# Kernel optimization log

Hardware: AMD Instinct MI355X
Metric: run time of the kernel (lower is better)

The kernel has to match this reference:

```python
import jax, jax.numpy as jnp
import numpy as np

N_NODES = 50000


def setup_inputs() -> dict:
    key = jax.random.key(0)
    ks = jax.random.split(key, 9)
    d = 256
    E = 800000
    inp = {
        "x": jax.random.normal(ks[0], (N_NODES, d), dtype=jnp.float32),
        "edge_index": jax.random.randint(ks[1], (2, E), 0, N_NODES, dtype=jnp.int64),
    }
    # 3 GCNConv layers, each: weight [in, out] and bias [out] (Glorot-ish scale)
    scale = 1.0 / np.sqrt(d)
    for i in range(3):
        inp[f"W{i+1}"] = jax.random.normal(ks[2 + 2 * i], (d, d), dtype=jnp.float32) * scale
        inp[f"b{i+1}"] = jnp.zeros((d,), dtype=jnp.float32)
    return inp


def _gcn_conv(h, src, dst, norm, W, b, n_nodes):
    # linear transform then normalized gather-scatter aggregation
    h = h @ W                                   # [N, out]
    msg = h[src] * norm[:, None]                # [E+N, out]
    out = jax.ops.segment_sum(msg, dst, num_segments=n_nodes)
    return out + b


def reference(x, edge_index, W1, b1, W2, b2, W3, b3):
    n = x.shape[0]
    loop = jnp.arange(n, dtype=edge_index.dtype)
    src = jnp.concatenate([edge_index[0], loop])  # add self-loops
    dst = jnp.concatenate([edge_index[1], loop])
    # symmetric normalization: deg^{-1/2}[src] * deg^{-1/2}[dst]
    deg = jax.ops.segment_sum(jnp.ones_like(dst, dtype=x.dtype), dst, num_segments=n)
    dinv = jnp.where(deg > 0, jax.lax.rsqrt(deg), 0.0)
    norm = dinv[src] * dinv[dst]

    h = _gcn_conv(x, src, dst, norm, W1, b1, n)
    h = jax.nn.relu(h)
    h = _gcn_conv(h, src, dst, norm, W2, b2, n)
    h = jax.nn.relu(h)
    h = _gcn_conv(h, src, dst, norm, W3, b3, n)
    return h
```

## Files before the change

kernel.cpp:

```cpp
#include <hip/hip_runtime.h>
#include <math.h>


using f16x8   = __attribute__((ext_vector_type(8))) _Float16;
using ushort4v = __attribute__((ext_vector_type(4))) unsigned short;
using f32x4   = __attribute__((ext_vector_type(4))) float;
using half4   = __attribute__((ext_vector_type(4))) _Float16;

__device__ inline unsigned short f2h_bits(float v) {
    _Float16 h = (_Float16)v;
    union { _Float16 h; unsigned short u; } c; c.h = h;
    return c.u;
}


__global__ void hist_kernel(const int* __restrict__ dst, int E, int* __restrict__ cnt) {
    int e = blockIdx.x * blockDim.x + threadIdx.x;
    if (e < E) atomicAdd(&cnt[dst[e]], 1);
}

__global__ void scan_block_kernel(const int* __restrict__ in, int n,
                                  int* __restrict__ out, int* __restrict__ bsums) {
    __shared__ int s[256];
    int t = threadIdx.x;
    int i = blockIdx.x * 256 + t;
    s[t] = (i < n) ? in[i] : 0;
    __syncthreads();
    for (int off = 1; off < 256; off <<= 1) {
        int addv = (t >= off) ? s[t - off] : 0;
        __syncthreads();
        s[t] += addv;
        __syncthreads();
    }
    if (i < n) out[i] = s[t];
    if (t == 255) bsums[blockIdx.x] = s[255];
}

__global__ void scan_sums_kernel(int* __restrict__ bsums, int nb) {
    __shared__ int s[256];
    int t = threadIdx.x;
    s[t] = (t < nb) ? bsums[t] : 0;
    __syncthreads();
    for (int off = 1; off < 256; off <<= 1) {
        int addv = (t >= off) ? s[t - off] : 0;
        __syncthreads();
        s[t] += addv;
        __syncthreads();
    }
    if (t < nb) bsums[t] = s[t];
}

__global__ void scan_add_dinv_kernel(int* __restrict__ scn, int n, const int* __restrict__ bsums,
                                     const int* __restrict__ cnt, float* __restrict__ dinv,
                                     int* __restrict__ cursor) {
    int i = blockIdx.x * 256 + threadIdx.x;
    if (i < n) {
        int s = scn[i] + (blockIdx.x > 0 ? bsums[blockIdx.x - 1] : 0);
        scn[i] = s;
        int c = cnt[i];
        dinv[i] = rsqrtf((float)(c + 1));
        cursor[i] = s - c;
    }
}

__global__ void scatter_kernel(const int* __restrict__ src, const int* __restrict__ dst, int E,
                               const float* __restrict__ dinv, int* __restrict__ cursor,
                               int* __restrict__ ssrc, float* __restrict__ snorm) {
    int e = blockIdx.x * blockDim.x + threadIdx.x;
    if (e < E) {
        int s = src[e], d0 = dst[e];
        int pos = atomicAdd(&cursor[d0], 1);
        ssrc[pos] = s;
        snorm[pos] = dinv[s] * dinv[d0];
    }
}

__global__ __launch_bounds__(256) void wsplit3_kernel(const float* __restrict__ Wa,
                                                      const float* __restrict__ Wb,
                                                      const float* __restrict__ Wc,
                                                      unsigned short* __restrict__ Wsp) {
    __shared__ float t[64][65];
    int w = blockIdx.z;
    const float* W = (w == 0) ? Wa : (w == 1) ? Wb : Wc;
    int k0 = blockIdx.x * 64, n0 = blockIdx.y * 64;
    int tid = threadIdx.x;
    int r = tid >> 6, c = tid & 63;
#pragma unroll
    for (int i = 0; i < 16; ++i) {
        int kk = i * 4 + r;
        t[kk][c] = W[(size_t)(k0 + kk) * 256 + n0 + c];
    }
    __syncthreads();
    unsigned short* Hi = Wsp + (size_t)w * 131072;
    unsigned short* Lo = Hi + 65536;
#pragma unroll
    for (int i = 0; i < 16; ++i) {
        int nn = i * 4 + r;
        float v = t[c][nn];
        _Float16 hh = (_Float16)v;
        float rr = v - (float)hh;
        _Float16 ll = (_Float16)rr;
        union { _Float16 h; unsigned short u; } ch, cl; ch.h = hh; cl.h = ll;
        Hi[(size_t)(n0 + nn) * 256 + k0 + c] = ch.u;
        Lo[(size_t)(n0 + nn) * 256 + k0 + c] = cl.u;
    }
}

__global__ void xcast_kernel(const float* __restrict__ in, unsigned short* __restrict__ out16,
                             int total4) {
    int i = blockIdx.x * blockDim.x + threadIdx.x;
    int stride = gridDim.x * blockDim.x;
    for (; i < total4; i += stride) {
        float4 v = ((const float4*)in)[i];
        ushort4v o;
        o[0] = f2h_bits(v.x); o[1] = f2h_bits(v.y);
        o[2] = f2h_bits(v.z); o[3] = f2h_bits(v.w);
        ((ushort4v*)out16)[i] = o;
    }
}

__global__ __launch_bounds__(256) void gemm_f16_kernel(
        const unsigned short* __restrict__ Af, const unsigned short* __restrict__ Whf,
        const unsigned short* __restrict__ Wlf, unsigned short* __restrict__ C16, int M) {
    __shared__ unsigned short lds[24576];

    const int tid  = threadIdx.x;
    const int lane = tid & 63;
    const int wid  = tid >> 6;
    const int wr   = wid >> 1, wc = wid & 1;

    const int orig = blockIdx.x;
    const int xcd  = orig & 7;
    const int idx  = orig >> 3;
    const int wg   = (xcd < 6 ? xcd * 98 : 588 + (xcd - 6) * 97) + idx;
    const int mBase = (wg >> 1) * 128;
    const int nBase = (wg & 1) * 128;

    const int b0 = (lane ^ (lane >> 2) ^ (lane >> 4)) & 1;
    const int b1 = ((lane >> 1) ^ (lane >> 3)) & 1;
    const int b2 = ((lane >> 2) ^ (lane >> 4)) & 1;
    const int g  = (lane & 0x38) | (b2 << 2) | (b1 << 1) | b0;
    const int srow = g >> 2;
    const int skg  = g & 3;

    const unsigned short* cptr[6];
    int cdst[6];
#pragma unroll
    for (int i = 0; i < 6; ++i) {
        int c = wid * 6 + i;
        int a = c >> 3;
        int s = c & 7;
        const unsigned short* base = (a == 0) ? Af : (a == 1) ? Whf : Wlf;
        int rb = (a == 0) ? mBase : nBase;
        int r = rb + s * 16 + srow;
        if (a == 0 && r >= M) r = M - 1;
        cptr[i] = base + (size_t)r * 256 + skg * 8;
        cdst[i] = a * 4096 + s * 512;
    }

    f32x4 acc[4][4];
#pragma unroll
    for (int i = 0; i < 4; ++i)
#pragma unroll
        for (int j = 0; j < 4; ++j) acc[i][j] = (f32x4){0.f, 0.f, 0.f, 0.f};

    auto stage = [&](int p, int k) {
        unsigned short* dbase = lds + p * 12288;
        const int k0 = k * 32;
#pragma unroll
        for (int i = 0; i < 6; ++i) {
            __builtin_amdgcn_global_load_lds(
                (const __attribute__((address_space(1))) void*)(cptr[i] + k0),
                (__attribute__((address_space(3))) void*)(dbase + cdst[i]),
                16, 0, 0);
        }
    };

    stage(0, 0);

#pragma unroll
    for (int k = 0; k < 8; ++k) {
        const int p = k & 1;
        if (k < 7) {
            stage(p ^ 1, k + 1);
            asm volatile("s_waitcnt vmcnt(6)" ::: "memory");
        } else {
            asm volatile("s_waitcnt vmcnt(0)" ::: "memory");
        }
        __builtin_amdgcn_s_barrier();

        const unsigned short* As = lds + p * 12288;
        const unsigned short* Bh = As + 4096;
        const unsigned short* Bl = As + 8192;

        const int kb = (lane >> 4) * 8;
        f16x8 fa[4], fbh[4], fbl[4];
#pragma unroll
        for (int mi = 0; mi < 4; ++mi) {
            int row = wr * 64 + mi * 16 + (lane & 15);
            int off = (row * 64 + kb * 2) ^ ((row & 7) << 4);
            fa[mi] = *(const f16x8*)((const char*)As + off);
        }
#pragma unroll
        for (int ni = 0; ni < 4; ++ni) {
            int col = wc * 64 + ni * 16 + (lane & 15);
            int off = (col * 64 + kb * 2) ^ ((col & 7) << 4);
            fbh[ni] = *(const f16x8*)((const char*)Bh + off);
            fbl[ni] = *(const f16x8*)((const char*)Bl + off);
        }
#pragma unroll
        for (int mi = 0; mi < 4; ++mi)
#pragma unroll
            for (int ni = 0; ni < 4; ++ni) {
                acc[mi][ni] = __builtin_amdgcn_mfma_f32_16x16x32_f16(
                    fa[mi], fbh[ni], acc[mi][ni], 0, 0, 0);
                acc[mi][ni] = __builtin_amdgcn_mfma_f32_16x16x32_f16(
                    fa[mi], fbl[ni], acc[mi][ni], 0, 0, 0);
            }
        __builtin_amdgcn_s_barrier();
    }

#pragma unroll
    for (int mi = 0; mi < 4; ++mi) {
        int row0 = mBase + wr * 64 + mi * 16 + (lane >> 4) * 4;
#pragma unroll
        for (int ni = 0; ni < 4; ++ni) {
            int col = nBase + wc * 64 + ni * 16 + (lane & 15);
#pragma unroll
            for (int r = 0; r < 4; ++r) {
                int row = row0 + r;
                if (row < M) C16[(size_t)row * 256 + col] = f2h_bits(acc[mi][ni][r]);
            }
        }
    }
}

template <int RELU, int SPLIT>
__global__ __launch_bounds__(256) void agg_kernel(const unsigned short* __restrict__ hH,
                                                  const int* __restrict__ ssrc,
                                                  const float* __restrict__ snorm,
                                                  const int* __restrict__ cnt,
                                                  const int* __restrict__ scanv,
                                                  const float* __restrict__ dinv,
                                                  const float* __restrict__ bias,
                                                  unsigned short* __restrict__ outH,
                                                  float* __restrict__ outF, int n) {
    int node = blockIdx.x * 4 + (threadIdx.x >> 6);
    int lane = threadIdx.x & 63;
    if (node >= n) return;
    int end = scanv[node];
    int start = end - cnt[node];
    float di = dinv[node];
    float wself = di * di;

    half4 v = ((const half4*)(hH + (size_t)node * 256))[lane];
    float ax = (float)v[0] * wself, ay = (float)v[1] * wself;
    float az = (float)v[2] * wself, aw = (float)v[3] * wself;

    int j = start;
    for (; j + 4 <= end; j += 4) {
        int s0 = ssrc[j], s1 = ssrc[j + 1], s2 = ssrc[j + 2], s3 = ssrc[j + 3];
        float w0 = snorm[j], w1 = snorm[j + 1], w2 = snorm[j + 2], w3 = snorm[j + 3];
        half4 u0 = ((const half4*)(hH + (size_t)s0 * 256))[lane];
        half4 u1 = ((const half4*)(hH + (size_t)s1 * 256))[lane];
        half4 u2 = ((const half4*)(hH + (size_t)s2 * 256))[lane];
        half4 u3 = ((const half4*)(hH + (size_t)s3 * 256))[lane];
        ax = fmaf((float)u0[0], w0, ax); ay = fmaf((float)u0[1], w0, ay);
        az = fmaf((float)u0[2], w0, az); aw = fmaf((float)u0[3], w0, aw);
        ax = fmaf((float)u1[0], w1, ax); ay = fmaf((float)u1[1], w1, ay);
        az = fmaf((float)u1[2], w1, az); aw = fmaf((float)u1[3], w1, aw);
        ax = fmaf((float)u2[0], w2, ax); ay = fmaf((float)u2[1], w2, ay);
        az = fmaf((float)u2[2], w2, az); aw = fmaf((float)u2[3], w2, aw);
        ax = fmaf((float)u3[0], w3, ax); ay = fmaf((float)u3[1], w3, ay);
        az = fmaf((float)u3[2], w3, az); aw = fmaf((float)u3[3], w3, aw);
    }
    for (; j < end; ++j) {
        int s = ssrc[j];
        float wn = snorm[j];
        half4 u = ((const half4*)(hH + (size_t)s * 256))[lane];
        ax = fmaf((float)u[0], wn, ax); ay = fmaf((float)u[1], wn, ay);
        az = fmaf((float)u[2], wn, az); aw = fmaf((float)u[3], wn, aw);
    }

    float4 bb = ((const float4*)bias)[lane];
    ax += bb.x; ay += bb.y; az += bb.z; aw += bb.w;
    if (RELU) {
        ax = fmaxf(ax, 0.0f); ay = fmaxf(ay, 0.0f);
        az = fmaxf(az, 0.0f); aw = fmaxf(aw, 0.0f);
    }
    if (SPLIT) {
        ushort4v o;
        o[0] = f2h_bits(ax); o[1] = f2h_bits(ay);
        o[2] = f2h_bits(az); o[3] = f2h_bits(aw);
        ((ushort4v*)(outH + (size_t)node * 256))[lane] = o;
    } else {
        float4 o = {ax, ay, az, aw};
        ((float4*)(outF + (size_t)node * 256))[lane] = o;
    }
}

extern "C" void kernel_launch(void* const* d_in, const int* in_sizes, int n_in,
                              void* d_out, int out_size, void* d_ws, size_t ws_size,
                              hipStream_t stream) {
    const float* x  = (const float*)d_in[0];
    const int*   ei = (const int*)d_in[1];
    const float* W1 = (const float*)d_in[2];
    const float* b1 = (const float*)d_in[3];
    const float* W2 = (const float*)d_in[4];
    const float* b2 = (const float*)d_in[5];
    const float* W3 = (const float*)d_in[6];
    const float* b3 = (const float*)d_in[7];

    const int n = in_sizes[0] / 256;
    const int E = in_sizes[1] / 2;
    const int* src = ei;
    const int* dst = ei + E;

    unsigned short* hAct = (unsigned short*)d_out;
    unsigned short* xF   = hAct + (size_t)n * 256;
    float* outF = (float*)d_out;

    char* ws = (char*)d_ws;
    unsigned short* hLin = (unsigned short*)ws;
    size_t off  = (size_t)n * 256 * 2;
    off = (off + 255) & ~(size_t)255;
    float* dinv = (float*)(ws + off); off += (size_t)n * 4;
    int*   cnt  = (int*)(ws + off);   off += (size_t)n * 4;
    int*   scn  = (int*)(ws + off);   off += (size_t)n * 4;
    int*   cur  = (int*)(ws + off);   off += (size_t)n * 4;
    int*   bsum = (int*)(ws + off);   off += 4096;
    int*   ssrc = (int*)(ws + off);   off += (size_t)E * 4;
    float* snrm = (float*)(ws + off); off += (size_t)E * 4;
    off = (off + 255) & ~(size_t)255;
    unsigned short* Wsp = (unsigned short*)(ws + off);
    off += (size_t)3 * 2 * 65536 * 2;

    hipMemsetAsync(cnt, 0, (size_t)n * 4, stream);

    const int eb = (E + 255) / 256;
    const int nb = (n + 255) / 256;

    wsplit3_kernel<<<dim3(4, 4, 3), 256, 0, stream>>>(W1, W2, W3, Wsp);
    xcast_kernel<<<2048, 256, 0, stream>>>(x, xF, n * 64);

    hist_kernel<<<eb, 256, 0, stream>>>(dst, E, cnt);
    scan_block_kernel<<<nb, 256, 0, stream>>>(cnt, n, scn, bsum);
    scan_sums_kernel<<<1, 256, 0, stream>>>(bsum, nb);
    scan_add_dinv_kernel<<<nb, 256, 0, stream>>>(scn, n, bsum, cnt, dinv, cur);
    scatter_kernel<<<eb, 256, 0, stream>>>(src, dst, E, dinv, cur, ssrc, snrm);

    const int gb = ((n + 127) / 128) * 2;
    const int ab = (n + 3) / 4;

    gemm_f16_kernel<<<gb, 256, 0, stream>>>(xF, Wsp, Wsp + 65536, hLin, n);
    agg_kernel<1, 1><<<ab, 256, 0, stream>>>(hLin, ssrc, snrm, cnt, scn, dinv, b1,
                                             hAct, nullptr, n);
    gemm_f16_kernel<<<gb, 256, 0, stream>>>(hAct, Wsp + 131072, Wsp + 196608, hLin, n);
    agg_kernel<1, 1><<<ab, 256, 0, stream>>>(hLin, ssrc, snrm, cnt, scn, dinv, b2,
                                             hAct, nullptr, n);
    gemm_f16_kernel<<<gb, 256, 0, stream>>>(hAct, Wsp + 262144, Wsp + 327680, hLin, n);
    agg_kernel<0, 0><<<ab, 256, 0, stream>>>(hLin, ssrc, snrm, cnt, scn, dinv, b3,
                                             nullptr, outF, n);
}
```

Measured before the change: 355.1 us.

## Widen GEMM tile to full 256 output columns with 512-thread blocks

The f16 GEMM now uses 512-thread blocks that each compute a 128x256 output tile covering all output columns. Each A tile is loaded once rather than twice across two N-halves. LDS per stage grows to hold the full split-precision weight slab. The XCD-aware block remapping is dropped, and the grid halves to 391 blocks, which reduces parallelism and may lower occupancy on the GPU.

```diff
diff --git a/kernel.cpp b/kernel.cpp
--- a/kernel.cpp
+++ b/kernel.cpp
@@ -119,22 +119,17 @@
     }
 }
 
-__global__ __launch_bounds__(256) void gemm_f16_kernel(
+__global__ __launch_bounds__(512) void gemm_f16_kernel(
         const unsigned short* __restrict__ Af, const unsigned short* __restrict__ Whf,
         const unsigned short* __restrict__ Wlf, unsigned short* __restrict__ C16, int M) {
-    __shared__ unsigned short lds[24576];
+    __shared__ unsigned short lds[40960];
 
     const int tid  = threadIdx.x;
     const int lane = tid & 63;
     const int wid  = tid >> 6;
-    const int wr   = wid >> 1, wc = wid & 1;
-
-    const int orig = blockIdx.x;
-    const int xcd  = orig & 7;
-    const int idx  = orig >> 3;
-    const int wg   = (xcd < 6 ? xcd * 98 : 588 + (xcd - 6) * 97) + idx;
-    const int mBase = (wg >> 1) * 128;
-    const int nBase = (wg & 1) * 128;
+    const int wr   = wid >> 2;
+    const int wc   = wid & 3;
+    const int mBase = blockIdx.x * 128;
 
     const int b0 = (lane ^ (lane >> 2) ^ (lane >> 4)) & 1;
     const int b1 = ((lane >> 1) ^ (lane >> 3)) & 1;
@@ -143,19 +138,29 @@
     const int srow = g >> 2;
     const int skg  = g & 3;
 
-    const unsigned short* cptr[6];
-    int cdst[6];
-#pragma unroll
-    for (int i = 0; i < 6; ++i) {
-        int c = wid * 6 + i;
-        int a = c >> 3;
-        int s = c & 7;
-        const unsigned short* base = (a == 0) ? Af : (a == 1) ? Whf : Wlf;
-        int rb = (a == 0) ? mBase : nBase;
-        int r = rb + s * 16 + srow;
-        if (a == 0 && r >= M) r = M - 1;
-        cptr[i] = base + (size_t)r * 256 + skg * 8;
-        cdst[i] = a * 4096 + s * 512;
+    const unsigned short* cptr[5];
+    int cdst[5];
+#pragma unroll
+    for (int i = 0; i < 5; ++i) {
+        int c = wid * 5 + i;
+        const unsigned short* base;
+        int row, dst;
+        if (c < 8) {
+            base = Af;
+            row = mBase + c * 16 + srow;
+            if (row >= M) row = M - 1;
+            dst = c * 512;
+        } else if (c < 24) {
+            base = Whf;
+            row = (c - 8) * 16 + srow;
+            dst = 4096 + (c - 8) * 512;
+        } else {
+            base = Wlf;
+            row = (c - 24) * 16 + srow;
+            dst = 12288 + (c - 24) * 512;
+        }
+        cptr[i] = base + (size_t)row * 256 + skg * 8;
+        cdst[i] = dst;
     }
 
     f32x4 acc[4][4];
@@ -165,10 +170,10 @@
         for (int j = 0; j < 4; ++j) acc[i][j] = (f32x4){0.f, 0.f, 0.f, 0.f};
 
     auto stage = [&](int p, int k) {
-        unsigned short* dbase = lds + p * 12288;
+        unsigned short* dbase = lds + p * 20480;
         const int k0 = k * 32;
 #pragma unroll
-        for (int i = 0; i < 6; ++i) {
+        for (int i = 0; i < 5; ++i) {
             __builtin_amdgcn_global_load_lds(
                 (const __attribute__((address_space(1))) void*)(cptr[i] + k0),
                 (__attribute__((address_space(3))) void*)(dbase + cdst[i]),
@@ -183,15 +188,15 @@
         const int p = k & 1;
         if (k < 7) {
             stage(p ^ 1, k + 1);
-            asm volatile("s_waitcnt vmcnt(6)" ::: "memory");
+            asm volatile("s_waitcnt vmcnt(5)" ::: "memory");
         } else {
             asm volatile("s_waitcnt vmcnt(0)" ::: "memory");
         }
         __builtin_amdgcn_s_barrier();
 
-        const unsigned short* As = lds + p * 12288;
+        const unsigned short* As = lds + p * 20480;
         const unsigned short* Bh = As + 4096;
-        const unsigned short* Bl = As + 8192;
+        const unsigned short* Bl = As + 12288;
 
         const int kb = (lane >> 4) * 8;
         f16x8 fa[4], fbh[4], fbl[4];
@@ -225,7 +230,7 @@
         int row0 = mBase + wr * 64 + mi * 16 + (lane >> 4) * 4;
 #pragma unroll
         for (int ni = 0; ni < 4; ++ni) {
-            int col = nBase + wc * 64 + ni * 16 + (lane & 15);
+            int col = wc * 64 + ni * 16 + (lane & 15);
 #pragma unroll
             for (int r = 0; r < 4; ++r) {
                 int row = row0 + r;
@@ -349,16 +354,16 @@
     scan_add_dinv_kernel<<<nb, 256, 0, stream>>>(scn, n, bsum, cnt, dinv, cur);
     scatter_kernel<<<eb, 256, 0, stream>>>(src, dst, E, dinv, cur, ssrc, snrm);
 
-    const int gb = ((n + 127) / 128) * 2;
+    const int gb = (n + 127) / 128;
     const int ab = (n + 3) / 4;
 
-    gemm_f16_kernel<<<gb, 256, 0, stream>>>(xF, Wsp, Wsp + 65536, hLin, n);
+    gemm_f16_kernel<<<gb, 512, 0, stream>>>(xF, Wsp, Wsp + 65536, hLin, n);
     agg_kernel<1, 1><<<ab, 256, 0, stream>>>(hLin, ssrc, snrm, cnt, scn, dinv, b1,
                                              hAct, nullptr, n);
-    gemm_f16_kernel<<<gb, 256, 0, stream>>>(hAct, Wsp + 131072, Wsp + 196608, hLin, n);
+    gemm_f16_kernel<<<gb, 512, 0, stream>>>(hAct, Wsp + 131072, Wsp + 196608, hLin, n);
     agg_kernel<1, 1><<<ab, 256, 0, stream>>>(hLin, ssrc, snrm, cnt, scn, dinv, b2,
                                              hAct, nullptr, n);
-    gemm_f16_kernel<<<gb, 256, 0, stream>>>(hAct, Wsp + 262144, Wsp + 327680, hLin, n);
+    gemm_f16_kernel<<<gb, 512, 0, stream>>>(hAct, Wsp + 262144, Wsp + 327680, hLin, n);
     agg_kernel<0, 0><<<ab, 256, 0, stream>>>(hLin, ssrc, snrm, cnt, scn, dinv, b3,
                                              nullptr, outF, n);
 }
```

After: 359.9 us. No clear change (+1.3%).
